# Kernel optimization log

Measured on AMD Instinct MI355X. Metric: run time of the kernel, lower is better.

The kernel has to match this reference:

```python
import jax, jax.numpy as jnp
import numpy as np

N, D, K, P = 4096, 256, 16, 3
MAXDEG = K + 1          # self loop guarantees deg >= 1, randint caps deg <= K+1
TAU, LAM, BETA, MARGIN = 0.8, 0.5, 1.0, 0.1
EPS_PD = 1e-6           # F.pairwise_distance eps (added to the difference)


def _make_adj(k):
    nbr = jax.random.randint(k, (N, K), 0, N)
    m = jnp.zeros((N, N), jnp.float32)
    m = m.at[jnp.arange(N)[:, None], nbr].set(1.0)
    m = m.at[jnp.arange(N), jnp.arange(N)].set(1.0)
    return m / m.sum(1, keepdims=True)  # row-normalized metapath adjacency


def setup_inputs():
    key = jax.random.key(0)
    ks = jax.random.split(key, 12)
    g = 1.414 * (2.0 / (D + D)) ** 0.5  # xavier_normal gain=1.414
    return {
        "h": jax.random.normal(ks[0], (N, D), jnp.float32),
        "mps": jnp.stack([_make_adj(ks[1 + i]) for i in range(P)]),
        "W_gcn": jax.random.normal(ks[4], (P, D, D), jnp.float32) * g,
        "b_gcn": jnp.zeros((P, D), jnp.float32),
        "prelu_a": jnp.full((P,), 0.25, jnp.float32),
        "att_fc_W": jax.random.normal(ks[5], (D, D), jnp.float32) * g,
        "att_fc_b": jnp.zeros((D,), jnp.float32),
        "att_vec": jax.random.normal(ks[6], (D,), jnp.float32) * g,
        "proj_W1": jax.random.normal(ks[7], (D, D), jnp.float32) * g,
        "proj_b1": jnp.zeros((D,), jnp.float32),
        "proj_W2": jax.random.normal(ks[8], (D, D), jnp.float32) * g,
        "proj_b2": jnp.zeros((D,), jnp.float32),
    }


def _gcn(h, adj, W, b, a):
    out = adj @ (h @ W.T) + b          # spmm(adj, fc(h)) + bias
    return jnp.where(out > 0, out, a * out)  # PReLU


def _node_loss(emb, adj):
    # vectorized form of the per-node nonzero/pairwise_distance loop
    mask = adj > 0                      # [N, N]
    deg = mask.sum(1)                   # [N], >= 1 via self loops
    # stable argsort: neighbors first (ascending index), matching torch.nonzero order
    pos_idx = jnp.argsort(~mask, axis=1)[:, :MAXDEG]
    neg_idx = jnp.argsort(mask, axis=1)[:, :MAXDEG]   # first deg non-neighbors
    anc = emb[:, None, :]               # anchor expanded over pairs
    dp = jnp.sum((anc - emb[pos_idx] + EPS_PD) ** 2, -1)  # [N, MAXDEG]
    dn = jnp.sum((anc - emb[neg_idx] + EPS_PD) ** 2, -1)
    valid = jnp.arange(MAXDEG)[None, :] < deg[:, None]
    per = jnp.maximum(dp - dn + MARGIN, 0.0) * valid
    return jnp.sum(per.sum(1) / deg.astype(emb.dtype))  # per-node mean, summed


def _proj(z, W1, b1, W2, b2):
    return jax.nn.elu(z @ W1.T + b1) @ W2.T + b2


def _contrast(z1, z2, pos, W1, b1, W2, b2):
    p1 = _proj(z1, W1, b1, W2, b2)
    p2 = _proj(z2, W1, b1, W2, b2)
    n1 = jnp.linalg.norm(p1, axis=-1, keepdims=True)
    n2 = jnp.linalg.norm(p2, axis=-1, keepdims=True)
    sim = jnp.exp((p1 @ p2.T) / (n1 * n2.T) / TAU)     # [N, N]
    m12 = sim / (sim.sum(1, keepdims=True) + 1e-8)
    m21 = sim.T / (sim.T.sum(1, keepdims=True) + 1e-8)
    l12 = -jnp.log((m12 * pos).sum(-1)).mean()
    l21 = -jnp.log((m21 * pos).sum(-1)).mean()
    return LAM * l12 + (1.0 - LAM) * l21


def reference(h, mps, W_gcn, b_gcn, prelu_a, att_fc_W, att_fc_b, att_vec,
              proj_W1, proj_b1, proj_W2, proj_b2):
    embeds = [_gcn(h, mps[i], W_gcn[i], b_gcn[i], prelu_a[i]) for i in range(P)]
    node_loss = sum(_node_loss(embeds[i], mps[i]) for i in range(P))
    # faithful to original control flow: i==0 inner loop overwrites self.loss,
    # so only the (0, P-1) pair survives from i==0
    closs = _contrast(embeds[0], embeds[P - 1], mps[0], proj_W1, proj_b1, proj_W2, proj_b2)
    for i in range(1, P - 1):
        for j in range(i + 1, P):
            closs = closs + _contrast(embeds[i], embeds[j], mps[i], proj_W1, proj_b1, proj_W2, proj_b2)
    # semantic attention over metapaths
    sp = jnp.stack([jnp.tanh(e @ att_fc_W.T + att_fc_b).mean(0) for e in embeds])  # [P, D]
    beta = jax.nn.softmax(sp @ att_vec)                                            # [P]
    z_mp = jnp.einsum('p,pnd->nd', beta, jnp.stack(embeds))
    return z_mp, node_loss + BETA * closs
```

## Files before the change

kernel.cpp:

```cpp
#include <hip/hip_runtime.h>
#include <hip/hip_bf16.h>

constexpr int N = 4096;
constexpr int D = 256;
constexpr int P = 3;
constexpr int MAXDEG = 17;
constexpr float TAU = 0.8f;
constexpr float MARGIN = 0.1f;
constexpr float EPS_PD = 1e-6f;

constexpr int LDP = 40;

constexpr int OFF_H    = 0;
constexpr int OFF_WG   = 1048576;
constexpr int OFF_ATTW = 1245184;
constexpr int OFF_W1   = 1310720;
constexpr int OFF_W2   = 1376256;
constexpr int OFF_BG   = 1441792;
constexpr int OFF_ATTB = 1442560;
constexpr int OFF_AV   = 1442816;
constexpr int OFF_PA   = 1443072;
constexpr int OFF_B1   = 1443328;
constexpr int OFF_B2   = 1443584;
constexpr int CONV_TOTAL = 1443840;

typedef __attribute__((ext_vector_type(8))) short bfrag8;
typedef __attribute__((ext_vector_type(4))) float facc4;

__device__ inline facc4 mfma16(bfrag8 a, bfrag8 b, facc4 c) {
    return __builtin_amdgcn_mfma_f32_16x16x32_bf16(a, b, c, 0, 0, 0);
}
__device__ inline float b2f(__hip_bfloat16 v) { return __bfloat162float(v); }
__device__ inline float bfbits2f(unsigned short u) {
    return __uint_as_float(((unsigned int)u) << 16);
}
__device__ inline unsigned short f2bfbits(float v) {
    __hip_bfloat16 t = __float2bfloat16(v);
    return *(unsigned short*)&t;
}
__device__ inline int get_bf(const int* __restrict__ counter) { return counter[0] > 100; }

__device__ inline float load_in(const void* p, size_t i, int bf) {
    return bf ? __bfloat162float(((const __hip_bfloat16*)p)[i])
              : ((const float*)p)[i];
}

__device__ __forceinline__ void gl_lds16(const __hip_bfloat16* g, __hip_bfloat16* l) {
    __builtin_amdgcn_global_load_lds(
        (const __attribute__((address_space(1))) unsigned int*)g,
        (__attribute__((address_space(3))) unsigned int*)l, 16, 0, 0);
}

__global__ void detect_dtype(const unsigned int* __restrict__ w, int nwords,
                             int* __restrict__ counter,
                             float* __restrict__ zbuf, int nz) {
    int t0 = blockIdx.x * blockDim.x + threadIdx.x;
    if (t0 < nz) zbuf[t0] = 0.f;
    int stride = gridDim.x * blockDim.x;
    int c = 0;
    for (int i = t0; i < nwords; i += stride) {
        unsigned int x = w[i];
        if ((x & 0xFFFF0000u) == 0u && x != 0u) c++;
    }
    for (int s = 32; s > 0; s >>= 1) c += __shfl_down(c, s);
    if ((threadIdx.x & 63) == 0 && c > 0) atomicMax(counter, 1 << 20);
}

__global__ void convert_all(const void* h, const void* wg, const void* attw,
                            const void* w1, const void* w2, const void* bg,
                            const void* attb, const void* av, const void* pa,
                            const void* b1, const void* b2,
                            const int* __restrict__ counter,
                            __hip_bfloat16* __restrict__ dst) {
    int bf = get_bf(counter);
    const void* srcs[11] = {h, wg, attw, w1, w2, bg, attb, av, pa, b1, b2};
    const int offs[11] = {OFF_H, OFF_WG, OFF_ATTW, OFF_W1, OFF_W2, OFF_BG,
                          OFF_ATTB, OFF_AV, OFF_PA, OFF_B1, OFF_B2};
    const int lens[11] = {1048576, 196608, 65536, 65536, 65536, 768, 256, 256, 3, 256, 256};
    int stride = gridDim.x * blockDim.x;
    int t0 = blockIdx.x * blockDim.x + threadIdx.x;
    #pragma unroll
    for (int s = 0; s < 11; s++) {
        for (int i = t0; i < lens[s]; i += stride)
            dst[offs[s] + i] = __float2bfloat16(load_in(srcs[s], i, bf));
    }
}

__global__ void extract_sparse(const void* __restrict__ mps, const int* __restrict__ counter,
                               int* __restrict__ nbr_idx, float* __restrict__ nbr_val,
                               int* __restrict__ neg_idx, int* __restrict__ deg) {
    int bf = get_bf(counter);
    int row = blockIdx.x;
    int t = threadIdx.x;
    __shared__ int cnt;
    __shared__ int sidx[32];
    __shared__ float sval[32];
    if (t == 0) cnt = 0;
    __syncthreads();
    int e0 = t * 16;
    if (bf) {
        const uint4* base = (const uint4*)((const __hip_bfloat16*)mps + (size_t)row * N + e0);
        #pragma unroll
        for (int v = 0; v < 2; v++) {
            uint4 w = base[v];
            unsigned int ws[4] = {w.x, w.y, w.z, w.w};
            #pragma unroll
            for (int j = 0; j < 4; j++) {
                unsigned short lo = (unsigned short)(ws[j] & 0xFFFFu);
                unsigned short hi = (unsigned short)(ws[j] >> 16);
                if (lo) { int k = atomicAdd(&cnt, 1); if (k < 32) { sidx[k] = e0 + v * 8 + j * 2;     sval[k] = bfbits2f(lo); } }
                if (hi) { int k = atomicAdd(&cnt, 1); if (k < 32) { sidx[k] = e0 + v * 8 + j * 2 + 1; sval[k] = bfbits2f(hi); } }
            }
        }
    } else {
        const float4* base = (const float4*)((const float*)mps + (size_t)row * N + e0);
        #pragma unroll
        for (int v = 0; v < 4; v++) {
            float4 w = base[v];
            float ws[4] = {w.x, w.y, w.z, w.w};
            #pragma unroll
            for (int j = 0; j < 4; j++)
                if (ws[j] > 0.f) { int k = atomicAdd(&cnt, 1); if (k < 32) { sidx[k] = e0 + v * 4 + j; sval[k] = ws[j]; } }
        }
    }
    __syncthreads();
    if (t < 64) {
        int dg = cnt; if (dg > MAXDEG) dg = MAXDEG;
        int myidx = 0; float myval = 0.f; int rank = 0;
        if (t < dg) {
            myidx = sidx[t]; myval = sval[t];
            for (int j = 0; j < dg; j++) rank += (sidx[j] < myidx) ? 1 : 0;
        }
        if (t < dg) { sidx[rank] = myidx; sval[rank] = myval; }
        if (t < MAXDEG) {
            nbr_idx[(size_t)row * MAXDEG + t] = (t < dg) ? sidx[t] : 0;
            nbr_val[(size_t)row * MAXDEG + t] = (t < dg) ? sval[t] : 0.f;
        }
        if (t == 0) deg[row] = dg;
        int c = t;
        bool cand = (c < dg + MAXDEG);
        bool isnbr = false;
        if (cand) for (int j = 0; j < dg; j++) isnbr |= (sidx[j] == c);
        bool nonnbr = cand && !isnbr;
        unsigned long long m = __ballot(nonnbr);
        int nrank = __popcll(m & ((c < 64) ? ((1ull << c) - 1ull) : ~0ull));
        if (nonnbr && nrank < MAXDEG) neg_idx[(size_t)row * MAXDEG + nrank] = c;
    }
}

__global__ void gemm_triple(const __hip_bfloat16* __restrict__ conv,
                            __hip_bfloat16* __restrict__ xbuf) {
    const __hip_bfloat16* A = conv + OFF_H;
    __shared__ __align__(16) __hip_bfloat16 As[64 * LDP];
    __shared__ __align__(16) __hip_bfloat16 Bs[3][64 * LDP];
    int bm = blockIdx.x * 64, bn = blockIdx.y * 64;
    int tid = threadIdx.x, wave = tid >> 6, lane = tid & 63;
    int quad = lane >> 4, l15 = lane & 15;
    int wr = (wave & 1) * 32, wc = (wave >> 1) * 32;
    facc4 acc[3][2][2] = {};
    int sr = tid >> 2, kq = (tid & 3) * 8;
    for (int k0 = 0; k0 < D; k0 += 32) {
        *(bfrag8*)&As[sr * LDP + kq] = *(const bfrag8*)&A[(size_t)(bm + sr) * D + k0 + kq];
        #pragma unroll
        for (int z = 0; z < 3; z++)
            *(bfrag8*)&Bs[z][sr * LDP + kq] =
                *(const bfrag8*)&conv[OFF_WG + (size_t)z * D * D + (size_t)(bn + sr) * D + k0 + kq];
        __syncthreads();
        bfrag8 af[2];
        #pragma unroll
        for (int mi = 0; mi < 2; mi++)
            af[mi] = *(const bfrag8*)&As[(wr + mi * 16 + l15) * LDP + quad * 8];
        #pragma unroll
        for (int z = 0; z < 3; z++) {
            bfrag8 bfr[2];
            #pragma unroll
            for (int ni = 0; ni < 2; ni++)
                bfr[ni] = *(const bfrag8*)&Bs[z][(wc + ni * 16 + l15) * LDP + quad * 8];
            #pragma unroll
            for (int mi = 0; mi < 2; mi++)
                #pragma unroll
                for (int ni = 0; ni < 2; ni++)
                    acc[z][mi][ni] = mfma16(af[mi], bfr[ni], acc[z][mi][ni]);
        }
        __syncthreads();
    }
    #pragma unroll
    for (int z = 0; z < 3; z++)
        #pragma unroll
        for (int mi = 0; mi < 2; mi++)
            #pragma unroll
            for (int ni = 0; ni < 2; ni++) {
                int col = bn + wc + ni * 16 + l15;
                #pragma unroll
                for (int r = 0; r < 4; r++) {
                    int row = bm + wr + mi * 16 + quad * 4 + r;
                    xbuf[(size_t)z * N * D + (size_t)row * D + col] =
                        __float2bfloat16(acc[z][mi][ni][r]);
                }
            }
}

__global__ void gemm_dual(const __hip_bfloat16* __restrict__ embBase,
                          const __hip_bfloat16* __restrict__ conv,
                          __hip_bfloat16* __restrict__ xbuf,
                          float* __restrict__ spacc) {
    int z = blockIdx.z;
    const __hip_bfloat16* A = embBase + (size_t)z * N * D;
    const __hip_bfloat16* Ba = conv + OFF_ATTW;
    const __hip_bfloat16* Bw = conv + OFF_W1;
    __shared__ __align__(16) __hip_bfloat16 As[64 * LDP];
    __shared__ __align__(16) __hip_bfloat16 Bsa[64 * LDP];
    __shared__ __align__(16) __hip_bfloat16 Bsw[64 * LDP];
    int bm = blockIdx.x * 64, bn = blockIdx.y * 64;
    int tid = threadIdx.x, wave = tid >> 6, lane = tid & 63;
    int quad = lane >> 4, l15 = lane & 15;
    int wr = (wave & 1) * 32, wc = (wave >> 1) * 32;
    facc4 accA[2][2] = {};
    facc4 accW[2][2] = {};
    int sr = tid >> 2, kq = (tid & 3) * 8;
    for (int k0 = 0; k0 < D; k0 += 32) {
        *(bfrag8*)&As[sr * LDP + kq]  = *(const bfrag8*)&A[(size_t)(bm + sr) * D + k0 + kq];
        *(bfrag8*)&Bsa[sr * LDP + kq] = *(const bfrag8*)&Ba[(size_t)(bn + sr) * D + k0 + kq];
        *(bfrag8*)&Bsw[sr * LDP + kq] = *(const bfrag8*)&Bw[(size_t)(bn + sr) * D + k0 + kq];
        __syncthreads();
        bfrag8 af[2], ba[2], bw[2];
        #pragma unroll
        for (int mi = 0; mi < 2; mi++)
            af[mi] = *(const bfrag8*)&As[(wr + mi * 16 + l15) * LDP + quad * 8];
        #pragma unroll
        for (int ni = 0; ni < 2; ni++) {
            ba[ni] = *(const bfrag8*)&Bsa[(wc + ni * 16 + l15) * LDP + quad * 8];
            bw[ni] = *(const bfrag8*)&Bsw[(wc + ni * 16 + l15) * LDP + quad * 8];
        }
        #pragma unroll
        for (int mi = 0; mi < 2; mi++)
            #pragma unroll
            for (int ni = 0; ni < 2; ni++) {
                accA[mi][ni] = mfma16(af[mi], ba[ni], accA[mi][ni]);
                accW[mi][ni] = mfma16(af[mi], bw[ni], accW[mi][ni]);
            }
        __syncthreads();
    }
    float cs[2] = {0.f, 0.f};
    #pragma unroll
    for (int mi = 0; mi < 2; mi++) {
        #pragma unroll
        for (int ni = 0; ni < 2; ni++) {
            int col = bn + wc + ni * 16 + l15;
            float battb = b2f(conv[OFF_ATTB + col]);
            float bb1   = b2f(conv[OFF_B1 + col]);
            #pragma unroll
            for (int r = 0; r < 4; r++) {
                int row = bm + wr + mi * 16 + quad * 4 + r;
                cs[ni] += tanhf(accA[mi][ni][r] + battb);
                float v = accW[mi][ni][r] + bb1;
                v = v > 0.f ? v : expm1f(v);
                xbuf[(size_t)z * N * D + (size_t)row * D + col] = __float2bfloat16(v);
            }
        }
    }
    #pragma unroll
    for (int ni = 0; ni < 2; ni++) {
        float v = cs[ni];
        v += __shfl_xor(v, 16); v += __shfl_xor(v, 32);
        if (quad == 0) {
            int col = bn + wc + ni * 16 + l15;
            atomicAdd(&spacc[(size_t)z * D + col], v);
        }
    }
}

__global__ void gemm_w2_norm(const __hip_bfloat16* __restrict__ xbase,
                             const __hip_bfloat16* __restrict__ conv,
                             __hip_bfloat16* __restrict__ qbase) {
    int z = blockIdx.z;
    const __hip_bfloat16* A = xbase + (size_t)z * N * D;
    const __hip_bfloat16* B = conv + OFF_W2;
    __shared__ __align__(16) __hip_bfloat16 As[16 * LDP];
    __shared__ __align__(16) __hip_bfloat16 Bs[256 * LDP];
    __shared__ float sred[4][16];
    int bm = blockIdx.x * 16;
    int tid = threadIdx.x, wave = tid >> 6, lane = tid & 63;
    int quad = lane >> 4, l15 = lane & 15;
    int wc = wave * 64;
    facc4 acc[4] = {};
    for (int k0 = 0; k0 < D; k0 += 32) {
        if (tid < 64) {
            int r = tid >> 2, kq = (tid & 3) * 8;
            *(bfrag8*)&As[r * LDP + kq] = *(const bfrag8*)&A[(size_t)(bm + r) * D + k0 + kq];
        }
        #pragma unroll
        for (int i = 0; i < 4; i++) {
            int f = tid + 256 * i;
            int r = f >> 2, kq = (f & 3) * 8;
            *(bfrag8*)&Bs[r * LDP + kq] = *(const bfrag8*)&B[(size_t)r * D + k0 + kq];
        }
        __syncthreads();
        bfrag8 af = *(const bfrag8*)&As[l15 * LDP + quad * 8];
        #pragma unroll
        for (int ni = 0; ni < 4; ni++) {
            bfrag8 bf = *(const bfrag8*)&Bs[(wc + ni * 16 + l15) * LDP + quad * 8];
            acc[ni] = mfma16(af, bf, acc[ni]);
        }
        __syncthreads();
    }
    float vv[4][4];
    #pragma unroll
    for (int ni = 0; ni < 4; ni++) {
        float bb = b2f(conv[OFF_B2 + wc + ni * 16 + l15]);
        #pragma unroll
        for (int r = 0; r < 4; r++) vv[ni][r] = acc[ni][r] + bb;
    }
    #pragma unroll
    for (int r = 0; r < 4; r++) {
        float ss = vv[0][r] * vv[0][r] + vv[1][r] * vv[1][r] +
                   vv[2][r] * vv[2][r] + vv[3][r] * vv[3][r];
        ss += __shfl_xor(ss, 1); ss += __shfl_xor(ss, 2);
        ss += __shfl_xor(ss, 4); ss += __shfl_xor(ss, 8);
        if (l15 == 0) sred[wave][quad * 4 + r] = ss;
    }
    __syncthreads();
    #pragma unroll
    for (int r = 0; r < 4; r++) {
        int rl = quad * 4 + r;
        float ssum = sred[0][rl] + sred[1][rl] + sred[2][rl] + sred[3][rl];
        float inv = rsqrtf(ssum + 1e-30f);
        int row = bm + rl;
        #pragma unroll
        for (int ni = 0; ni < 4; ni++)
            qbase[(size_t)z * N * D + (size_t)row * D + wc + ni * 16 + l15] =
                __float2bfloat16(vv[ni][r] * inv);
    }
}

__global__ void spmm_prelu(const __hip_bfloat16* __restrict__ Xbase,
                           const int* __restrict__ nbr_idx, const float* __restrict__ nbr_val,
                           const int* __restrict__ deg, const __hip_bfloat16* __restrict__ conv,
                           __hip_bfloat16* __restrict__ embBase) {
    int z = blockIdx.z;
    int wave = threadIdx.x >> 6, lane = threadIdx.x & 63;
    int n = blockIdx.x * 4 + wave;
    const __hip_bfloat16* X = Xbase + (size_t)z * N * D;
    int dg = deg[z * N + n];
    int idxv = 0; float valv = 0.f;
    if (lane < MAXDEG) {
        idxv = nbr_idx[((size_t)z * N + n) * MAXDEG + lane];
        valv = nbr_val[((size_t)z * N + n) * MAXDEG + lane];
    }
    float acc[4] = {0.f, 0.f, 0.f, 0.f};
    int k = 0;
    for (; k + 3 < dg; k += 4) {
        int j0 = __shfl(idxv, k), j1 = __shfl(idxv, k + 1);
        int j2 = __shfl(idxv, k + 2), j3 = __shfl(idxv, k + 3);
        float v0 = __shfl(valv, k), v1 = __shfl(valv, k + 1);
        float v2 = __shfl(valv, k + 2), v3 = __shfl(valv, k + 3);
        ushort4 x0 = *(const ushort4*)&X[(size_t)j0 * D + lane * 4];
        ushort4 x1 = *(const ushort4*)&X[(size_t)j1 * D + lane * 4];
        ushort4 x2 = *(const ushort4*)&X[(size_t)j2 * D + lane * 4];
        ushort4 x3 = *(const ushort4*)&X[(size_t)j3 * D + lane * 4];
        acc[0] += v0 * bfbits2f(x0.x) + v1 * bfbits2f(x1.x) + v2 * bfbits2f(x2.x) + v3 * bfbits2f(x3.x);
        acc[1] += v0 * bfbits2f(x0.y) + v1 * bfbits2f(x1.y) + v2 * bfbits2f(x2.y) + v3 * bfbits2f(x3.y);
        acc[2] += v0 * bfbits2f(x0.z) + v1 * bfbits2f(x1.z) + v2 * bfbits2f(x2.z) + v3 * bfbits2f(x3.z);
        acc[3] += v0 * bfbits2f(x0.w) + v1 * bfbits2f(x1.w) + v2 * bfbits2f(x2.w) + v3 * bfbits2f(x3.w);
    }
    for (; k < dg; k++) {
        int j0 = __shfl(idxv, k); float v0 = __shfl(valv, k);
        ushort4 x0 = *(const ushort4*)&X[(size_t)j0 * D + lane * 4];
        acc[0] += v0 * bfbits2f(x0.x); acc[1] += v0 * bfbits2f(x0.y);
        acc[2] += v0 * bfbits2f(x0.z); acc[3] += v0 * bfbits2f(x0.w);
    }
    ushort4 bb = *(const ushort4*)&conv[OFF_BG + z * D + lane * 4];
    float a = b2f(conv[OFF_PA + z]);
    ushort4 o;
    float v0 = acc[0] + bfbits2f(bb.x); o.x = f2bfbits(v0 > 0.f ? v0 : a * v0);
    float v1 = acc[1] + bfbits2f(bb.y); o.y = f2bfbits(v1 > 0.f ? v1 : a * v1);
    float v2 = acc[2] + bfbits2f(bb.z); o.z = f2bfbits(v2 > 0.f ? v2 : a * v2);
    float v3 = acc[3] + bfbits2f(bb.w); o.w = f2bfbits(v3 > 0.f ? v3 : a * v3);
    *(ushort4*)&embBase[(size_t)z * N * D + (size_t)n * D + lane * 4] = o;
}

__global__ void sim_mfma(const __hip_bfloat16* __restrict__ q,
                         float* __restrict__ rowsum, float* __restrict__ colsum) {
    int pair = blockIdx.z;
    const __hip_bfloat16* Qa = q + (size_t)pair * N * D;
    const __hip_bfloat16* Qb = q + (size_t)2 * N * D;
    __shared__ __align__(16) __hip_bfloat16 As[128 * 64];
    __shared__ __align__(16) __hip_bfloat16 Bs[128 * 64];
    int bm = blockIdx.x * 128, bn = blockIdx.y * 128;
    int tid = threadIdx.x, wave = tid >> 6, lane = tid & 63;
    int quad = lane >> 4, l15 = lane & 15;
    int wr = (wave & 1) * 64, wc = (wave >> 1) * 64;
    facc4 acc[4][4] = {};
    int sr0 = tid >> 3;
    int cc  = tid & 7;
    for (int k0 = 0; k0 < D; k0 += 64) {
        #pragma unroll
        for (int i = 0; i < 4; i++) {
            int r = sr0 + 32 * i;
            int cg = (cc ^ (r & 7)) * 8;
            gl_lds16(&Qa[(size_t)(bm + r) * D + k0 + cg], &As[r * 64 + cc * 8]);
            gl_lds16(&Qb[(size_t)(bn + r) * D + k0 + cg], &Bs[r * 64 + cc * 8]);
        }
        __syncthreads();
        #pragma unroll
        for (int kk = 0; kk < 64; kk += 32) {
            int kb = kk >> 3;
            bfrag8 af[4], bfr[4];
            #pragma unroll
            for (int mi = 0; mi < 4; mi++) {
                int R = wr + mi * 16 + l15;
                int pc = ((kb + quad) ^ (l15 & 7)) * 8;
                af[mi] = *(const bfrag8*)&As[R * 64 + pc];
            }
            #pragma unroll
            for (int ni = 0; ni < 4; ni++) {
                int R = wc + ni * 16 + l15;
                int pc = ((kb + quad) ^ (l15 & 7)) * 8;
                bfr[ni] = *(const bfrag8*)&Bs[R * 64 + pc];
            }
            #pragma unroll
            for (int mi = 0; mi < 4; mi++)
                #pragma unroll
                for (int ni = 0; ni < 4; ni++)
                    acc[mi][ni] = mfma16(af[mi], bfr[ni], acc[mi][ni]);
        }
        __syncthreads();
    }
    constexpr float invtau = 1.0f / TAU;
    float rs[4][4];
    float cs[4] = {0.f, 0.f, 0.f, 0.f};
    #pragma unroll
    for (int mi = 0; mi < 4; mi++)
        #pragma unroll
        for (int r = 0; r < 4; r++) rs[mi][r] = 0.f;
    #pragma unroll
    for (int mi = 0; mi < 4; mi++)
        #pragma unroll
        for (int ni = 0; ni < 4; ni++)
            #pragma unroll
            for (int r = 0; r < 4; r++) {
                float e = __expf(acc[mi][ni][r] * invtau);
                rs[mi][r] += e;
                cs[ni] += e;
            }
    #pragma unroll
    for (int mi = 0; mi < 4; mi++)
        #pragma unroll
        for (int r = 0; r < 4; r++) {
            float v = rs[mi][r];
            v += __shfl_xor(v, 1); v += __shfl_xor(v, 2);
            v += __shfl_xor(v, 4); v += __shfl_xor(v, 8);
            rs[mi][r] = v;
        }
    if (l15 == 0) {
        #pragma unroll
        for (int mi = 0; mi < 4; mi++)
            #pragma unroll
            for (int r = 0; r < 4; r++)
                atomicAdd(&rowsum[(size_t)pair * N + bm + wr + mi * 16 + quad * 4 + r], rs[mi][r]);
    }
    #pragma unroll
    for (int ni = 0; ni < 4; ni++) {
        float v = cs[ni];
        v += __shfl_xor(v, 16); v += __shfl_xor(v, 32);
        if (quad == 0)
            atomicAdd(&colsum[(size_t)pair * N + bn + wc + ni * 16 + l15], v);
    }
}

__global__ void edge_losses(const __hip_bfloat16* __restrict__ embBase,
                            const __hip_bfloat16* __restrict__ q,
                            const int* __restrict__ nbr_idx, const float* __restrict__ nbr_val,
                            const int* __restrict__ neg_idx, const int* __restrict__ deg,
                            float* __restrict__ nlpart,
                            float* __restrict__ pdrow, float* __restrict__ pdcol) {
    int z = blockIdx.z;
    int wave = threadIdx.x >> 6, lane = threadIdx.x & 63;
    int n = blockIdx.x * 4 + wave;
    if (z < P) {
        const __hip_bfloat16* emb = embBase + (size_t)z * N * D;
        int dg = deg[z * N + n];
        int ipv = 0, igv = 0;
        if (lane < MAXDEG) {
            ipv = nbr_idx[((size_t)z * N + n) * MAXDEG + lane];
            igv = neg_idx[((size_t)z * N + n) * MAXDEG + lane];
        }
        ushort4 ar = *(const ushort4*)&emb[(size_t)n * D + lane * 4];
        float a[4] = {bfbits2f(ar.x), bfbits2f(ar.y), bfbits2f(ar.z), bfbits2f(ar.w)};
        float s = 0.f;
        int k = 0;
        for (; k + 1 < dg; k += 2) {
            int jp0 = __shfl(ipv, k), jn0 = __shfl(igv, k);
            int jp1 = __shfl(ipv, k + 1), jn1 = __shfl(igv, k + 1);
            ushort4 pr0 = *(const ushort4*)&emb[(size_t)jp0 * D + lane * 4];
            ushort4 nr0 = *(const ushort4*)&emb[(size_t)jn0 * D + lane * 4];
            ushort4 pr1 = *(const ushort4*)&emb[(size_t)jp1 * D + lane * 4];
            ushort4 nr1 = *(const ushort4*)&emb[(size_t)jn1 * D + lane * 4];
            float dp0, dn0, dp1, dn1;
            {
                float x0 = a[0] - bfbits2f(pr0.x) + EPS_PD, y0 = a[0] - bfbits2f(nr0.x) + EPS_PD;
                float x1 = a[1] - bfbits2f(pr0.y) + EPS_PD, y1 = a[1] - bfbits2f(nr0.y) + EPS_PD;
                float x2 = a[2] - bfbits2f(pr0.z) + EPS_PD, y2 = a[2] - bfbits2f(nr0.z) + EPS_PD;
                float x3 = a[3] - bfbits2f(pr0.w) + EPS_PD, y3 = a[3] - bfbits2f(nr0.w) + EPS_PD;
                dp0 = x0 * x0 + x1 * x1 + x2 * x2 + x3 * x3;
                dn0 = y0 * y0 + y1 * y1 + y2 * y2 + y3 * y3;
            }
            {
                float x0 = a[0] - bfbits2f(pr1.x) + EPS_PD, y0 = a[0] - bfbits2f(nr1.x) + EPS_PD;
                float x1 = a[1] - bfbits2f(pr1.y) + EPS_PD, y1 = a[1] - bfbits2f(nr1.y) + EPS_PD;
                float x2 = a[2] - bfbits2f(pr1.z) + EPS_PD, y2 = a[2] - bfbits2f(nr1.z) + EPS_PD;
                float x3 = a[3] - bfbits2f(pr1.w) + EPS_PD, y3 = a[3] - bfbits2f(nr1.w) + EPS_PD;
                dp1 = x0 * x0 + x1 * x1 + x2 * x2 + x3 * x3;
                dn1 = y0 * y0 + y1 * y1 + y2 * y2 + y3 * y3;
            }
            #pragma unroll
            for (int st = 1; st <= 32; st <<= 1) {
                dp0 += __shfl_xor(dp0, st); dn0 += __shfl_xor(dn0, st);
                dp1 += __shfl_xor(dp1, st); dn1 += __shfl_xor(dn1, st);
            }
            float v0 = dp0 - dn0 + MARGIN; s += v0 > 0.f ? v0 : 0.f;
            float v1 = dp1 - dn1 + MARGIN; s += v1 > 0.f ? v1 : 0.f;
        }
        if (k < dg) {
            int jp = __shfl(ipv, k), jn = __shfl(igv, k);
            ushort4 pr = *(const ushort4*)&emb[(size_t)jp * D + lane * 4];
            ushort4 nr = *(const ushort4*)&emb[(size_t)jn * D + lane * 4];
            float x0 = a[0] - bfbits2f(pr.x) + EPS_PD, y0 = a[0] - bfbits2f(nr.x) + EPS_PD;
            float x1 = a[1] - bfbits2f(pr.y) + EPS_PD, y1 = a[1] - bfbits2f(nr.y) + EPS_PD;
            float x2 = a[2] - bfbits2f(pr.z) + EPS_PD, y2 = a[2] - bfbits2f(nr.z) + EPS_PD;
            float x3 = a[3] - bfbits2f(pr.w) + EPS_PD, y3 = a[3] - bfbits2f(nr.w) + EPS_PD;
            float dp = x0 * x0 + x1 * x1 + x2 * x2 + x3 * x3;
            float dn = y0 * y0 + y1 * y1 + y2 * y2 + y3 * y3;
            #pragma unroll
            for (int st = 1; st <= 32; st <<= 1) { dp += __shfl_xor(dp, st); dn += __shfl_xor(dn, st); }
            float v = dp - dn + MARGIN;
            s += v > 0.f ? v : 0.f;
        }
        if (lane == 0) nlpart[z * N + n] = s / (float)dg;
    } else {
        int pair = z - P;
        const __hip_bfloat16* Qa = q + (size_t)pair * N * D;
        const __hip_bfloat16* Qb = q + (size_t)2 * N * D;
        int dg = deg[pair * N + n];
        int idxv = 0; float valv = 0.f;
        if (lane < MAXDEG) {
            idxv = nbr_idx[((size_t)pair * N + n) * MAXDEG + lane];
            valv = nbr_val[((size_t)pair * N + n) * MAXDEG + lane];
        }
        const float invtau = 1.0f / TAU;
        ushort4 ar = *(const ushort4*)&Qa[(size_t)n * D + lane * 4];
        ushort4 br = *(const ushort4*)&Qb[(size_t)n * D + lane * 4];
        float a[4] = {bfbits2f(ar.x), bfbits2f(ar.y), bfbits2f(ar.z), bfbits2f(ar.w)};
        float b[4] = {bfbits2f(br.x), bfbits2f(br.y), bfbits2f(br.z), bfbits2f(br.w)};
        float sr = 0.f, sc = 0.f;
        int k = 0;
        for (; k + 1 < dg; k += 2) {
            int j0 = __shfl(idxv, k), j1 = __shfl(idxv, k + 1);
            float vk0 = __shfl(valv, k), vk1 = __shfl(valv, k + 1);
            ushort4 pj0 = *(const ushort4*)&Qb[(size_t)j0 * D + lane * 4];
            ushort4 aj0 = *(const ushort4*)&Qa[(size_t)j0 * D + lane * 4];
            ushort4 pj1 = *(const ushort4*)&Qb[(size_t)j1 * D + lane * 4];
            ushort4 aj1 = *(const ushort4*)&Qa[(size_t)j1 * D + lane * 4];
            float dr0 = a[0] * bfbits2f(pj0.x) + a[1] * bfbits2f(pj0.y) +
                        a[2] * bfbits2f(pj0.z) + a[3] * bfbits2f(pj0.w);
            float dc0 = b[0] * bfbits2f(aj0.x) + b[1] * bfbits2f(aj0.y) +
                        b[2] * bfbits2f(aj0.z) + b[3] * bfbits2f(aj0.w);
            float dr1 = a[0] * bfbits2f(pj1.x) + a[1] * bfbits2f(pj1.y) +
                        a[2] * bfbits2f(pj1.z) + a[3] * bfbits2f(pj1.w);
            float dc1 = b[0] * bfbits2f(aj1.x) + b[1] * bfbits2f(aj1.y) +
                        b[2] * bfbits2f(aj1.z) + b[3] * bfbits2f(aj1.w);
            #pragma unroll
            for (int s2 = 1; s2 <= 32; s2 <<= 1) {
                dr0 += __shfl_xor(dr0, s2); dc0 += __shfl_xor(dc0, s2);
                dr1 += __shfl_xor(dr1, s2); dc1 += __shfl_xor(dc1, s2);
            }
            sr += __expf(dr0 * invtau) * vk0 + __expf(dr1 * invtau) * vk1;
            sc += __expf(dc0 * invtau) * vk0 + __expf(dc1 * invtau) * vk1;
        }
        if (k < dg) {
            int j = __shfl(idxv, k);
            float vk = __shfl(valv, k);
            ushort4 pj = *(const ushort4*)&Qb[(size_t)j * D + lane * 4];
            ushort4 aj = *(const ushort4*)&Qa[(size_t)j * D + lane * 4];
            float dr = a[0] * bfbits2f(pj.x) + a[1] * bfbits2f(pj.y) +
                       a[2] * bfbits2f(pj.z) + a[3] * bfbits2f(pj.w);
            float dc = b[0] * bfbits2f(aj.x) + b[1] * bfbits2f(aj.y) +
                       b[2] * bfbits2f(aj.z) + b[3] * bfbits2f(aj.w);
            #pragma unroll
            for (int s2 = 1; s2 <= 32; s2 <<= 1) { dr += __shfl_xor(dr, s2); dc += __shfl_xor(dc, s2); }
            sr += __expf(dr * invtau) * vk;
            sc += __expf(dc * invtau) * vk;
        }
        if (lane == 0) { pdrow[pair * N + n] = sr; pdcol[pair * N + n] = sc; }
    }
}

__global__ void finalize(const float* __restrict__ nlpart,
                         const float* __restrict__ rowsum, const float* __restrict__ colsum,
                         const float* __restrict__ pdrow, const float* __restrict__ pdcol,
                         const float* __restrict__ spacc,
                         const __hip_bfloat16* __restrict__ conv,
                         const __hip_bfloat16* __restrict__ embBase,
                         const int* __restrict__ counter,
                         void* __restrict__ out) {
    int bf = get_bf(counter);
    int t = threadIdx.x;
    __shared__ float red[256];
    if (blockIdx.x == 0) {
        float s = 0.f;
        for (int i = t; i < P * N; i += 256) s += nlpart[i];
        for (int i = t; i < 2 * N; i += 256) {
            float l12 = -logf(pdrow[i] / (rowsum[i] + 1e-8f));
            float l21 = -logf(pdcol[i] / (colsum[i] + 1e-8f));
            s += (0.5f * l12 + 0.5f * l21) / (float)N;
        }
        red[t] = s;
        __syncthreads();
        for (int st = 128; st > 0; st >>= 1) { if (t < st) red[t] += red[t + st]; __syncthreads(); }
        if (t == 0) {
            if (bf) ((__hip_bfloat16*)out)[(size_t)N * D] = __float2bfloat16(red[0]);
            else    ((float*)out)[(size_t)N * D] = red[0];
        }
        return;
    }
    __shared__ float w[P];
    for (int p = 0; p < P; p++) {
        float v = (spacc[p * D + t] / (float)N) * b2f(conv[OFF_AV + t]);
        red[t] = v;
        __syncthreads();
        for (int s = 128; s > 0; s >>= 1) { if (t < s) red[t] += red[t + s]; __syncthreads(); }
        if (t == 0) w[p] = red[0];
        __syncthreads();
    }
    float m = fmaxf(w[0], fmaxf(w[1], w[2]));
    float e0 = __expf(w[0] - m), e1 = __expf(w[1] - m), e2 = __expf(w[2] - m);
    float ssum = e0 + e1 + e2;
    float b0 = e0 / ssum, b1 = e1 / ssum, b2 = e2 / ssum;
    int slice = blockIdx.x - 1;
    int base = slice * (N * D / 64);
    for (int e = t * 4; e < N * D / 64; e += 256 * 4) {
        int i = base + e;
        ushort4 x0 = *(const ushort4*)&embBase[i];
        ushort4 x1 = *(const ushort4*)&embBase[(size_t)N * D + i];
        ushort4 x2 = *(const ushort4*)&embBase[(size_t)2 * N * D + i];
        float v[4];
        v[0] = b0 * bfbits2f(x0.x) + b1 * bfbits2f(x1.x) + b2 * bfbits2f(x2.x);
        v[1] = b0 * bfbits2f(x0.y) + b1 * bfbits2f(x1.y) + b2 * bfbits2f(x2.y);
        v[2] = b0 * bfbits2f(x0.z) + b1 * bfbits2f(x1.z) + b2 * bfbits2f(x2.z);
        v[3] = b0 * bfbits2f(x0.w) + b1 * bfbits2f(x1.w) + b2 * bfbits2f(x2.w);
        if (bf) {
            ushort4 ov;
            ov.x = f2bfbits(v[0]); ov.y = f2bfbits(v[1]);
            ov.z = f2bfbits(v[2]); ov.w = f2bfbits(v[3]);
            *(ushort4*)&((__hip_bfloat16*)out)[i] = ov;
        } else {
            float* o = (float*)out;
            o[i] = v[0]; o[i + 1] = v[1]; o[i + 2] = v[2]; o[i + 3] = v[3];
        }
    }
}

extern "C" void kernel_launch(void* const* d_in, const int* in_sizes, int n_in,
                              void* d_out, int out_size, void* d_ws, size_t ws_size,
                              hipStream_t stream) {
    const void* h        = d_in[0];
    const void* mps      = d_in[1];
    const void* W_gcn    = d_in[2];
    const void* b_gcn    = d_in[3];
    const void* prelu_a  = d_in[4];
    const void* att_fc_W = d_in[5];
    const void* att_fc_b = d_in[6];
    const void* att_vec  = d_in[7];
    const void* proj_W1  = d_in[8];
    const void* proj_b1  = d_in[9];
    const void* proj_W2  = d_in[10];
    const void* proj_b2  = d_in[11];

    char* ws = (char*)d_ws;
    size_t off = 0;
    auto alloc = [&](size_t bytes) -> char* {
        char* p = ws + off;
        off = (off + bytes + 255) & ~(size_t)255;
        return p;
    };
    __hip_bfloat16* conv = (__hip_bfloat16*)alloc((size_t)CONV_TOTAL * 2);
    __hip_bfloat16* xbuf = (__hip_bfloat16*)alloc((size_t)P * N * D * 2);
    __hip_bfloat16* emb  = (__hip_bfloat16*)alloc((size_t)P * N * D * 2);
    __hip_bfloat16* q    = (__hip_bfloat16*)alloc((size_t)P * N * D * 2);
    int*   nbr_idx = (int*)alloc((size_t)P * N * MAXDEG * 4);
    float* nbr_val = (float*)alloc((size_t)P * N * MAXDEG * 4);
    int*   neg_idx = (int*)alloc((size_t)P * N * MAXDEG * 4);
    int*   deg     = (int*)alloc((size_t)P * N * 4);
    float* nlpart  = (float*)alloc((size_t)P * N * 4);
    float* pdrow   = (float*)alloc((size_t)2 * N * 4);
    float* pdcol   = (float*)alloc((size_t)2 * N * 4);
    char* zero_begin = ws + off;
    float* rowsum = (float*)alloc((size_t)2 * N * 4);
    float* colsum = (float*)alloc((size_t)2 * N * 4);
    float* spacc  = (float*)alloc((size_t)P * D * 4);
    size_t zero_bytes = (size_t)((ws + off) - zero_begin);
    int*   counter = (int*)alloc(16);

    detect_dtype<<<1024, 256, 0, stream>>>((const unsigned int*)mps, 2 * 1024 * 1024,
                                           counter, (float*)zero_begin,
                                           (int)(zero_bytes / 4));

    convert_all<<<512, 256, 0, stream>>>(h, W_gcn, att_fc_W, proj_W1, proj_W2, b_gcn,
                                         att_fc_b, att_vec, prelu_a, proj_b1, proj_b2,
                                         counter, conv);

    extract_sparse<<<P * N, 256, 0, stream>>>(mps, counter, nbr_idx, nbr_val, neg_idx, deg);

    gemm_triple<<<dim3(N / 64, D / 64), 256, 0, stream>>>(conv, xbuf);
    spmm_prelu<<<dim3(N / 4, 1, P), 256, 0, stream>>>(xbuf, nbr_idx, nbr_val, deg, conv, emb);
    gemm_dual<<<dim3(N / 64, D / 64, P), 256, 0, stream>>>(emb, conv, xbuf, spacc);
    gemm_w2_norm<<<dim3(N / 16, 1, P), 256, 0, stream>>>(xbuf, conv, q);
    sim_mfma<<<dim3(N / 128, N / 128, 2), 256, 0, stream>>>(q, rowsum, colsum);
    edge_losses<<<dim3(N / 4, 1, P + 2), 256, 0, stream>>>(emb, q, nbr_idx, nbr_val,
                                                           neg_idx, deg, nlpart, pdrow, pdcol);
    finalize<<<65, 256, 0, stream>>>(nlpart, rowsum, colsum, pdrow, pdcol,
                                     spacc, conv, emb, counter, d_out);
}
```

Baseline: 472.2 us.

## Fuse independent stages into shared launches to cut kernel count

The standalone convert pass is removed. The first GEMM now reads h and W_gcn directly and converts fp32 to bf16 on the fly, and it runs in the same launch as the sparse-extraction blocks using blockIdx ranges. The node-loss computation moves into the dual GEMM launch as extra blocks. The similarity GEMM, positive-pair sums and z_mp mixing are merged into one launch, leaving a small loss-finalize kernel. This removes several launches and inter-kernel bubbles and lets independent work overlap, at the cost of heterogeneous blocks with shared-memory sizing set by the largest branch.

```diff
diff --git a/kernel.cpp b/kernel.cpp
--- a/kernel.cpp
+++ b/kernel.cpp
@@ -66,270 +66,161 @@
     if ((threadIdx.x & 63) == 0 && c > 0) atomicMax(counter, 1 << 20);
 }
 
-__global__ void convert_all(const void* h, const void* wg, const void* attw,
-                            const void* w1, const void* w2, const void* bg,
-                            const void* attb, const void* av, const void* pa,
-                            const void* b1, const void* b2,
-                            const int* __restrict__ counter,
-                            __hip_bfloat16* __restrict__ dst) {
-    int bf = get_bf(counter);
-    const void* srcs[11] = {h, wg, attw, w1, w2, bg, attb, av, pa, b1, b2};
-    const int offs[11] = {OFF_H, OFF_WG, OFF_ATTW, OFF_W1, OFF_W2, OFF_BG,
-                          OFF_ATTB, OFF_AV, OFF_PA, OFF_B1, OFF_B2};
-    const int lens[11] = {1048576, 196608, 65536, 65536, 65536, 768, 256, 256, 3, 256, 256};
-    int stride = gridDim.x * blockDim.x;
-    int t0 = blockIdx.x * blockDim.x + threadIdx.x;
-    #pragma unroll
-    for (int s = 0; s < 11; s++) {
-        for (int i = t0; i < lens[s]; i += stride)
-            dst[offs[s] + i] = __float2bfloat16(load_in(srcs[s], i, bf));
-    }
-}
-
-__global__ void extract_sparse(const void* __restrict__ mps, const int* __restrict__ counter,
-                               int* __restrict__ nbr_idx, float* __restrict__ nbr_val,
-                               int* __restrict__ neg_idx, int* __restrict__ deg) {
-    int bf = get_bf(counter);
-    int row = blockIdx.x;
-    int t = threadIdx.x;
-    __shared__ int cnt;
-    __shared__ int sidx[32];
-    __shared__ float sval[32];
-    if (t == 0) cnt = 0;
-    __syncthreads();
-    int e0 = t * 16;
-    if (bf) {
-        const uint4* base = (const uint4*)((const __hip_bfloat16*)mps + (size_t)row * N + e0);
-        #pragma unroll
-        for (int v = 0; v < 2; v++) {
-            uint4 w = base[v];
-            unsigned int ws[4] = {w.x, w.y, w.z, w.w};
-            #pragma unroll
-            for (int j = 0; j < 4; j++) {
-                unsigned short lo = (unsigned short)(ws[j] & 0xFFFFu);
-                unsigned short hi = (unsigned short)(ws[j] >> 16);
-                if (lo) { int k = atomicAdd(&cnt, 1); if (k < 32) { sidx[k] = e0 + v * 8 + j * 2;     sval[k] = bfbits2f(lo); } }
-                if (hi) { int k = atomicAdd(&cnt, 1); if (k < 32) { sidx[k] = e0 + v * 8 + j * 2 + 1; sval[k] = bfbits2f(hi); } }
-            }
-        }
-    } else {
-        const float4* base = (const float4*)((const float*)mps + (size_t)row * N + e0);
-        #pragma unroll
-        for (int v = 0; v < 4; v++) {
-            float4 w = base[v];
-            float ws[4] = {w.x, w.y, w.z, w.w};
-            #pragma unroll
-            for (int j = 0; j < 4; j++)
-                if (ws[j] > 0.f) { int k = atomicAdd(&cnt, 1); if (k < 32) { sidx[k] = e0 + v * 4 + j; sval[k] = ws[j]; } }
-        }
-    }
-    __syncthreads();
-    if (t < 64) {
-        int dg = cnt; if (dg > MAXDEG) dg = MAXDEG;
-        int myidx = 0; float myval = 0.f; int rank = 0;
-        if (t < dg) {
-            myidx = sidx[t]; myval = sval[t];
-            for (int j = 0; j < dg; j++) rank += (sidx[j] < myidx) ? 1 : 0;
-        }
-        if (t < dg) { sidx[rank] = myidx; sval[rank] = myval; }
-        if (t < MAXDEG) {
-            nbr_idx[(size_t)row * MAXDEG + t] = (t < dg) ? sidx[t] : 0;
-            nbr_val[(size_t)row * MAXDEG + t] = (t < dg) ? sval[t] : 0.f;
-        }
-        if (t == 0) deg[row] = dg;
-        int c = t;
-        bool cand = (c < dg + MAXDEG);
-        bool isnbr = false;
-        if (cand) for (int j = 0; j < dg; j++) isnbr |= (sidx[j] == c);
-        bool nonnbr = cand && !isnbr;
-        unsigned long long m = __ballot(nonnbr);
-        int nrank = __popcll(m & ((c < 64) ? ((1ull << c) - 1ull) : ~0ull));
-        if (nonnbr && nrank < MAXDEG) neg_idx[(size_t)row * MAXDEG + nrank] = c;
-    }
-}
-
-__global__ void gemm_triple(const __hip_bfloat16* __restrict__ conv,
-                            __hip_bfloat16* __restrict__ xbuf) {
-    const __hip_bfloat16* A = conv + OFF_H;
+__global__ void stage2(const void* __restrict__ h, const void* __restrict__ wg,
+                       const void* __restrict__ mps,
+                       const void* attw, const void* w1, const void* w2,
+                       const void* bg, const void* attb, const void* av,
+                       const void* pa, const void* b1, const void* b2,
+                       const int* __restrict__ counter,
+                       __hip_bfloat16* __restrict__ conv,
+                       __hip_bfloat16* __restrict__ xbuf,
+                       int* __restrict__ nbr_idx, float* __restrict__ nbr_val,
+                       int* __restrict__ neg_idx, int* __restrict__ deg) {
     __shared__ __align__(16) __hip_bfloat16 As[64 * LDP];
     __shared__ __align__(16) __hip_bfloat16 Bs[3][64 * LDP];
-    int bm = blockIdx.x * 64, bn = blockIdx.y * 64;
-    int tid = threadIdx.x, wave = tid >> 6, lane = tid & 63;
-    int quad = lane >> 4, l15 = lane & 15;
-    int wr = (wave & 1) * 32, wc = (wave >> 1) * 32;
-    facc4 acc[3][2][2] = {};
-    int sr = tid >> 2, kq = (tid & 3) * 8;
-    for (int k0 = 0; k0 < D; k0 += 32) {
-        *(bfrag8*)&As[sr * LDP + kq] = *(const bfrag8*)&A[(size_t)(bm + sr) * D + k0 + kq];
+    int bid = blockIdx.x;
+    int bf = get_bf(counter);
+    if (bid < 256) {
+        int bm = (bid & 63) * 64, bn = (bid >> 6) * 64;
+        int tid = threadIdx.x, wave = tid >> 6, lane = tid & 63;
+        int quad = lane >> 4, l15 = lane & 15;
+        int wr = (wave & 1) * 32, wc = (wave >> 1) * 32;
+        facc4 acc[3][2][2] = {};
+        int sr = tid >> 2, kq = (tid & 3) * 8;
+        for (int k0 = 0; k0 < D; k0 += 32) {
+            if (bf) {
+                *(bfrag8*)&As[sr * LDP + kq] =
+                    *(const bfrag8*)((const unsigned short*)h + (size_t)(bm + sr) * D + k0 + kq);
+                #pragma unroll
+                for (int z = 0; z < 3; z++)
+                    *(bfrag8*)&Bs[z][sr * LDP + kq] =
+                        *(const bfrag8*)((const unsigned short*)wg +
+                                         (size_t)z * D * D + (size_t)(bn + sr) * D + k0 + kq);
+            } else {
+                const float* hp = (const float*)h + (size_t)(bm + sr) * D + k0 + kq;
+                float4 a0 = *(const float4*)hp, a1 = *(const float4*)(hp + 4);
+                bfrag8 t;
+                t[0] = f2bfbits(a0.x); t[1] = f2bfbits(a0.y);
+                t[2] = f2bfbits(a0.z); t[3] = f2bfbits(a0.w);
+                t[4] = f2bfbits(a1.x); t[5] = f2bfbits(a1.y);
+                t[6] = f2bfbits(a1.z); t[7] = f2bfbits(a1.w);
+                *(bfrag8*)&As[sr * LDP + kq] = t;
+                #pragma unroll
+                for (int z = 0; z < 3; z++) {
+                    const float* wp = (const float*)wg +
+                        (size_t)z * D * D + (size_t)(bn + sr) * D + k0 + kq;
+                    float4 b0 = *(const float4*)wp, b1v = *(const float4*)(wp + 4);
+                    bfrag8 u;
+                    u[0] = f2bfbits(b0.x);  u[1] = f2bfbits(b0.y);
+                    u[2] = f2bfbits(b0.z);  u[3] = f2bfbits(b0.w);
+                    u[4] = f2bfbits(b1v.x); u[5] = f2bfbits(b1v.y);
+                    u[6] = f2bfbits(b1v.z); u[7] = f2bfbits(b1v.w);
+                    *(bfrag8*)&Bs[z][sr * LDP + kq] = u;
+                }
+            }
+            __syncthreads();
+            bfrag8 af[2];
+            #pragma unroll
+            for (int mi = 0; mi < 2; mi++)
+                af[mi] = *(const bfrag8*)&As[(wr + mi * 16 + l15) * LDP + quad * 8];
+            #pragma unroll
+            for (int z = 0; z < 3; z++) {
+                bfrag8 bfr[2];
+                #pragma unroll
+                for (int ni = 0; ni < 2; ni++)
+                    bfr[ni] = *(const bfrag8*)&Bs[z][(wc + ni * 16 + l15) * LDP + quad * 8];
+                #pragma unroll
+                for (int mi = 0; mi < 2; mi++)
+                    #pragma unroll
+                    for (int ni = 0; ni < 2; ni++)
+                        acc[z][mi][ni] = mfma16(af[mi], bfr[ni], acc[z][mi][ni]);
+            }
+            __syncthreads();
+        }
         #pragma unroll
         for (int z = 0; z < 3; z++)
-            *(bfrag8*)&Bs[z][sr * LDP + kq] =
-                *(const bfrag8*)&conv[OFF_WG + (size_t)z * D * D + (size_t)(bn + sr) * D + k0 + kq];
+            #pragma unroll
+            for (int mi = 0; mi < 2; mi++)
+                #pragma unroll
+                for (int ni = 0; ni < 2; ni++) {
+                    int col = bn + wc + ni * 16 + l15;
+                    #pragma unroll
+                    for (int r = 0; r < 4; r++) {
+                        int row = bm + wr + mi * 16 + quad * 4 + r;
+                        xbuf[(size_t)z * N * D + (size_t)row * D + col] =
+                            __float2bfloat16(acc[z][mi][ni][r]);
+                    }
+                }
+    } else if (bid < 256 + P * N) {
+        int row = bid - 256;
+        int t = threadIdx.x;
+        int* cnt = (int*)As;
+        int* sidx = ((int*)As) + 1;
+        float* sval = (float*)(((int*)As) + 33);
+        if (t == 0) *cnt = 0;
         __syncthreads();
-        bfrag8 af[2];
-        #pragma unroll
-        for (int mi = 0; mi < 2; mi++)
-            af[mi] = *(const bfrag8*)&As[(wr + mi * 16 + l15) * LDP + quad * 8];
-        #pragma unroll
-        for (int z = 0; z < 3; z++) {
-            bfrag8 bfr[2];
-            #pragma unroll
-            for (int ni = 0; ni < 2; ni++)
-                bfr[ni] = *(const bfrag8*)&Bs[z][(wc + ni * 16 + l15) * LDP + quad * 8];
-            #pragma unroll
-            for (int mi = 0; mi < 2; mi++)
-                #pragma unroll
-                for (int ni = 0; ni < 2; ni++)
-                    acc[z][mi][ni] = mfma16(af[mi], bfr[ni], acc[z][mi][ni]);
+        int e0 = t * 16;
+        if (bf) {
+            const uint4* base = (const uint4*)((const __hip_bfloat16*)mps + (size_t)row * N + e0);
+            #pragma unroll
+            for (int v = 0; v < 2; v++) {
+                uint4 w = base[v];
+                unsigned int ws[4] = {w.x, w.y, w.z, w.w};
+                #pragma unroll
+                for (int j = 0; j < 4; j++) {
+                    unsigned short lo = (unsigned short)(ws[j] & 0xFFFFu);
+                    unsigned short hi = (unsigned short)(ws[j] >> 16);
+                    if (lo) { int k = atomicAdd(cnt, 1); if (k < 32) { sidx[k] = e0 + v * 8 + j * 2;     sval[k] = bfbits2f(lo); } }
+                    if (hi) { int k = atomicAdd(cnt, 1); if (k < 32) { sidx[k] = e0 + v * 8 + j * 2 + 1; sval[k] = bfbits2f(hi); } }
+                }
+            }
+        } else {
+            const float4* base = (const float4*)((const float*)mps + (size_t)row * N + e0);
+            #pragma unroll
+            for (int v = 0; v < 4; v++) {
+                float4 w = base[v];
+                float ws[4] = {w.x, w.y, w.z, w.w};
+                #pragma unroll
+                for (int j = 0; j < 4; j++)
+                    if (ws[j] > 0.f) { int k = atomicAdd(cnt, 1); if (k < 32) { sidx[k] = e0 + v * 4 + j; sval[k] = ws[j]; } }
+            }
         }
         __syncthreads();
-    }
-    #pragma unroll
-    for (int z = 0; z < 3; z++)
-        #pragma unroll
-        for (int mi = 0; mi < 2; mi++)
-            #pragma unroll
-            for (int ni = 0; ni < 2; ni++) {
-                int col = bn + wc + ni * 16 + l15;
-                #pragma unroll
-                for (int r = 0; r < 4; r++) {
-                    int row = bm + wr + mi * 16 + quad * 4 + r;
-                    xbuf[(size_t)z * N * D + (size_t)row * D + col] =
-                        __float2bfloat16(acc[z][mi][ni][r]);
-                }
-            }
-}
-
-__global__ void gemm_dual(const __hip_bfloat16* __restrict__ embBase,
-                          const __hip_bfloat16* __restrict__ conv,
-                          __hip_bfloat16* __restrict__ xbuf,
-                          float* __restrict__ spacc) {
-    int z = blockIdx.z;
-    const __hip_bfloat16* A = embBase + (size_t)z * N * D;
-    const __hip_bfloat16* Ba = conv + OFF_ATTW;
-    const __hip_bfloat16* Bw = conv + OFF_W1;
-    __shared__ __align__(16) __hip_bfloat16 As[64 * LDP];
-    __shared__ __align__(16) __hip_bfloat16 Bsa[64 * LDP];
-    __shared__ __align__(16) __hip_bfloat16 Bsw[64 * LDP];
-    int bm = blockIdx.x * 64, bn = blockIdx.y * 64;
-    int tid = threadIdx.x, wave = tid >> 6, lane = tid & 63;
-    int quad = lane >> 4, l15 = lane & 15;
-    int wr = (wave & 1) * 32, wc = (wave >> 1) * 32;
-    facc4 accA[2][2] = {};
-    facc4 accW[2][2] = {};
-    int sr = tid >> 2, kq = (tid & 3) * 8;
-    for (int k0 = 0; k0 < D; k0 += 32) {
-        *(bfrag8*)&As[sr * LDP + kq]  = *(const bfrag8*)&A[(size_t)(bm + sr) * D + k0 + kq];
-        *(bfrag8*)&Bsa[sr * LDP + kq] = *(const bfrag8*)&Ba[(size_t)(bn + sr) * D + k0 + kq];
-        *(bfrag8*)&Bsw[sr * LDP + kq] = *(const bfrag8*)&Bw[(size_t)(bn + sr) * D + k0 + kq];
-        __syncthreads();
-        bfrag8 af[2], ba[2], bw[2];
-        #pragma unroll
-        for (int mi = 0; mi < 2; mi++)
-            af[mi] = *(const bfrag8*)&As[(wr + mi * 16 + l15) * LDP + quad * 8];
-        #pragma unroll
-        for (int ni = 0; ni < 2; ni++) {
-            ba[ni] = *(const bfrag8*)&Bsa[(wc + ni * 16 + l15) * LDP + quad * 8];
-            bw[ni] = *(const bfrag8*)&Bsw[(wc + ni * 16 + l15) * LDP + quad * 8];
-        }
-        #pragma unroll
-        for (int mi = 0; mi < 2; mi++)
-            #pragma unroll
-            for (int ni = 0; ni < 2; ni++) {
-                accA[mi][ni] = mfma16(af[mi], ba[ni], accA[mi][ni]);
-                accW[mi][ni] = mfma16(af[mi], bw[ni], accW[mi][ni]);
-            }
-        __syncthreads();
-    }
-    float cs[2] = {0.f, 0.f};
-    #pragma unroll
-    for (int mi = 0; mi < 2; mi++) {
-        #pragma unroll
-        for (int ni = 0; ni < 2; ni++) {
-            int col = bn + wc + ni * 16 + l15;
-            float battb = b2f(conv[OFF_ATTB + col]);
-            float bb1   = b2f(conv[OFF_B1 + col]);
-            #pragma unroll
-            for (int r = 0; r < 4; r++) {
-                int row = bm + wr + mi * 16 + quad * 4 + r;
-                cs[ni] += tanhf(accA[mi][ni][r] + battb);
-                float v = accW[mi][ni][r] + bb1;
-                v = v > 0.f ? v : expm1f(v);
-                xbuf[(size_t)z * N * D + (size_t)row * D + col] = __float2bfloat16(v);
-            }
-        }
-    }
-    #pragma unroll
-    for (int ni = 0; ni < 2; ni++) {
-        float v = cs[ni];
-        v += __shfl_xor(v, 16); v += __shfl_xor(v, 32);
-        if (quad == 0) {
-            int col = bn + wc + ni * 16 + l15;
-            atomicAdd(&spacc[(size_t)z * D + col], v);
-        }
-    }
-}
-
-__global__ void gemm_w2_norm(const __hip_bfloat16* __restrict__ xbase,
-                             const __hip_bfloat16* __restrict__ conv,
-                             __hip_bfloat16* __restrict__ qbase) {
-    int z = blockIdx.z;
-    const __hip_bfloat16* A = xbase + (size_t)z * N * D;
-    const __hip_bfloat16* B = conv + OFF_W2;
-    __shared__ __align__(16) __hip_bfloat16 As[16 * LDP];
-    __shared__ __align__(16) __hip_bfloat16 Bs[256 * LDP];
-    __shared__ float sred[4][16];
-    int bm = blockIdx.x * 16;
-    int tid = threadIdx.x, wave = tid >> 6, lane = tid & 63;
-    int quad = lane >> 4, l15 = lane & 15;
-    int wc = wave * 64;
-    facc4 acc[4] = {};
-    for (int k0 = 0; k0 < D; k0 += 32) {
-        if (tid < 64) {
-            int r = tid >> 2, kq = (tid & 3) * 8;
-            *(bfrag8*)&As[r * LDP + kq] = *(const bfrag8*)&A[(size_t)(bm + r) * D + k0 + kq];
-        }
-        #pragma unroll
-        for (int i = 0; i < 4; i++) {
-            int f = tid + 256 * i;
-            int r = f >> 2, kq = (f & 3) * 8;
-            *(bfrag8*)&Bs[r * LDP + kq] = *(const bfrag8*)&B[(size_t)r * D + k0 + kq];
-        }
-        __syncthreads();
-        bfrag8 af = *(const bfrag8*)&As[l15 * LDP + quad * 8];
-        #pragma unroll
-        for (int ni = 0; ni < 4; ni++) {
-            bfrag8 bf = *(const bfrag8*)&Bs[(wc + ni * 16 + l15) * LDP + quad * 8];
-            acc[ni] = mfma16(af, bf, acc[ni]);
-        }
-        __syncthreads();
-    }
-    float vv[4][4];
-    #pragma unroll
-    for (int ni = 0; ni < 4; ni++) {
-        float bb = b2f(conv[OFF_B2 + wc + ni * 16 + l15]);
-        #pragma unroll
-        for (int r = 0; r < 4; r++) vv[ni][r] = acc[ni][r] + bb;
-    }
-    #pragma unroll
-    for (int r = 0; r < 4; r++) {
-        float ss = vv[0][r] * vv[0][r] + vv[1][r] * vv[1][r] +
-                   vv[2][r] * vv[2][r] + vv[3][r] * vv[3][r];
-        ss += __shfl_xor(ss, 1); ss += __shfl_xor(ss, 2);
-        ss += __shfl_xor(ss, 4); ss += __shfl_xor(ss, 8);
-        if (l15 == 0) sred[wave][quad * 4 + r] = ss;
-    }
-    __syncthreads();
-    #pragma unroll
-    for (int r = 0; r < 4; r++) {
-        int rl = quad * 4 + r;
-        float ssum = sred[0][rl] + sred[1][rl] + sred[2][rl] + sred[3][rl];
-        float inv = rsqrtf(ssum + 1e-30f);
-        int row = bm + rl;
-        #pragma unroll
-        for (int ni = 0; ni < 4; ni++)
-            qbase[(size_t)z * N * D + (size_t)row * D + wc + ni * 16 + l15] =
-                __float2bfloat16(vv[ni][r] * inv);
+        if (t < 64) {
+            int dg = *cnt; if (dg > MAXDEG) dg = MAXDEG;
+            int myidx = 0; float myval = 0.f; int rank = 0;
+            if (t < dg) {
+                myidx = sidx[t]; myval = sval[t];
+                for (int j = 0; j < dg; j++) rank += (sidx[j] < myidx) ? 1 : 0;
+            }
+            if (t < dg) { sidx[rank] = myidx; sval[rank] = myval; }
+            if (t < MAXDEG) {
+                nbr_idx[(size_t)row * MAXDEG + t] = (t < dg) ? sidx[t] : 0;
+                nbr_val[(size_t)row * MAXDEG + t] = (t < dg) ? sval[t] : 0.f;
+            }
+            if (t == 0) deg[row] = dg;
+            int c = t;
+            bool cand = (c < dg + MAXDEG);
+            bool isnbr = false;
+            if (cand) for (int j = 0; j < dg; j++) isnbr |= (sidx[j] == c);
+            bool nonnbr = cand && !isnbr;
+            unsigned long long m = __ballot(nonnbr);
+            int nrank = __popcll(m & ((c < 64) ? ((1ull << c) - 1ull) : ~0ull));
+            if (nonnbr && nrank < MAXDEG) neg_idx[(size_t)row * MAXDEG + nrank] = c;
+        }
+    } else {
+        int cb = bid - (256 + P * N);
+        const void* srcs[9] = {attw, w1, w2, bg, attb, av, pa, b1, b2};
+        const int offs[9] = {OFF_ATTW, OFF_W1, OFF_W2, OFF_BG, OFF_ATTB,
+                             OFF_AV, OFF_PA, OFF_B1, OFF_B2};
+        const int lens[9] = {65536, 65536, 65536, 768, 256, 256, 3, 256, 256};
+        int stride = 64 * 256;
+        int t0 = cb * 256 + threadIdx.x;
+        #pragma unroll
+        for (int s = 0; s < 9; s++) {
+            for (int i = t0; i < lens[s]; i += stride)
+                conv[offs[s] + i] = __float2bfloat16(load_in(srcs[s], i, bf));
+        }
     }
 }
 
@@ -379,105 +270,83 @@
     *(ushort4*)&embBase[(size_t)z * N * D + (size_t)n * D + lane * 4] = o;
 }
 
-__global__ void sim_mfma(const __hip_bfloat16* __restrict__ q,
-                         float* __restrict__ rowsum, float* __restrict__ colsum) {
-    int pair = blockIdx.z;
-    const __hip_bfloat16* Qa = q + (size_t)pair * N * D;
-    const __hip_bfloat16* Qb = q + (size_t)2 * N * D;
-    __shared__ __align__(16) __hip_bfloat16 As[128 * 64];
-    __shared__ __align__(16) __hip_bfloat16 Bs[128 * 64];
-    int bm = blockIdx.x * 128, bn = blockIdx.y * 128;
-    int tid = threadIdx.x, wave = tid >> 6, lane = tid & 63;
-    int quad = lane >> 4, l15 = lane & 15;
-    int wr = (wave & 1) * 64, wc = (wave >> 1) * 64;
-    facc4 acc[4][4] = {};
-    int sr0 = tid >> 3;
-    int cc  = tid & 7;
-    for (int k0 = 0; k0 < D; k0 += 64) {
-        #pragma unroll
-        for (int i = 0; i < 4; i++) {
-            int r = sr0 + 32 * i;
-            int cg = (cc ^ (r & 7)) * 8;
-            gl_lds16(&Qa[(size_t)(bm + r) * D + k0 + cg], &As[r * 64 + cc * 8]);
-            gl_lds16(&Qb[(size_t)(bn + r) * D + k0 + cg], &Bs[r * 64 + cc * 8]);
-        }
-        __syncthreads();
-        #pragma unroll
-        for (int kk = 0; kk < 64; kk += 32) {
-            int kb = kk >> 3;
-            bfrag8 af[4], bfr[4];
-            #pragma unroll
-            for (int mi = 0; mi < 4; mi++) {
-                int R = wr + mi * 16 + l15;
-                int pc = ((kb + quad) ^ (l15 & 7)) * 8;
-                af[mi] = *(const bfrag8*)&As[R * 64 + pc];
-            }
-            #pragma unroll
-            for (int ni = 0; ni < 4; ni++) {
-                int R = wc + ni * 16 + l15;
-                int pc = ((kb + quad) ^ (l15 & 7)) * 8;
-                bfr[ni] = *(const bfrag8*)&Bs[R * 64 + pc];
-            }
-            #pragma unroll
-            for (int mi = 0; mi < 4; mi++)
-                #pragma unroll
-                for (int ni = 0; ni < 4; ni++)
-                    acc[mi][ni] = mfma16(af[mi], bfr[ni], acc[mi][ni]);
-        }
-        __syncthreads();
-    }
-    constexpr float invtau = 1.0f / TAU;
-    float rs[4][4];
-    float cs[4] = {0.f, 0.f, 0.f, 0.f};
-    #pragma unroll
-    for (int mi = 0; mi < 4; mi++)
-        #pragma unroll
-        for (int r = 0; r < 4; r++) rs[mi][r] = 0.f;
-    #pragma unroll
-    for (int mi = 0; mi < 4; mi++)
-        #pragma unroll
-        for (int ni = 0; ni < 4; ni++)
-            #pragma unroll
-            for (int r = 0; r < 4; r++) {
-                float e = __expf(acc[mi][ni][r] * invtau);
-                rs[mi][r] += e;
-                cs[ni] += e;
-            }
-    #pragma unroll
-    for (int mi = 0; mi < 4; mi++)
-        #pragma unroll
-        for (int r = 0; r < 4; r++) {
-            float v = rs[mi][r];
-            v += __shfl_xor(v, 1); v += __shfl_xor(v, 2);
-            v += __shfl_xor(v, 4); v += __shfl_xor(v, 8);
-            rs[mi][r] = v;
-        }
-    if (l15 == 0) {
-        #pragma unroll
-        for (int mi = 0; mi < 4; mi++)
-            #pragma unroll
-            for (int r = 0; r < 4; r++)
-                atomicAdd(&rowsum[(size_t)pair * N + bm + wr + mi * 16 + quad * 4 + r], rs[mi][r]);
-    }
-    #pragma unroll
-    for (int ni = 0; ni < 4; ni++) {
-        float v = cs[ni];
-        v += __shfl_xor(v, 16); v += __shfl_xor(v, 32);
-        if (quad == 0)
-            atomicAdd(&colsum[(size_t)pair * N + bn + wc + ni * 16 + l15], v);
-    }
-}
-
-__global__ void edge_losses(const __hip_bfloat16* __restrict__ embBase,
-                            const __hip_bfloat16* __restrict__ q,
-                            const int* __restrict__ nbr_idx, const float* __restrict__ nbr_val,
-                            const int* __restrict__ neg_idx, const int* __restrict__ deg,
-                            float* __restrict__ nlpart,
-                            float* __restrict__ pdrow, float* __restrict__ pdcol) {
+__global__ void gemm_dual_nl(const __hip_bfloat16* __restrict__ embBase,
+                             const __hip_bfloat16* __restrict__ conv,
+                             __hip_bfloat16* __restrict__ xbuf,
+                             float* __restrict__ spacc,
+                             const int* __restrict__ nbr_idx,
+                             const int* __restrict__ neg_idx,
+                             const int* __restrict__ deg,
+                             float* __restrict__ nlpart) {
+    __shared__ __align__(16) __hip_bfloat16 As[64 * LDP];
+    __shared__ __align__(16) __hip_bfloat16 Bsa[64 * LDP];
+    __shared__ __align__(16) __hip_bfloat16 Bsw[64 * LDP];
     int z = blockIdx.z;
-    int wave = threadIdx.x >> 6, lane = threadIdx.x & 63;
-    int n = blockIdx.x * 4 + wave;
-    if (z < P) {
+    if (blockIdx.y < 4) {
+        const __hip_bfloat16* A = embBase + (size_t)z * N * D;
+        const __hip_bfloat16* Ba = conv + OFF_ATTW;
+        const __hip_bfloat16* Bw = conv + OFF_W1;
+        int bm = blockIdx.x * 64, bn = blockIdx.y * 64;
+        int tid = threadIdx.x, wave = tid >> 6, lane = tid & 63;
+        int quad = lane >> 4, l15 = lane & 15;
+        int wr = (wave & 1) * 32, wc = (wave >> 1) * 32;
+        facc4 accA[2][2] = {};
+        facc4 accW[2][2] = {};
+        int sr = tid >> 2, kq = (tid & 3) * 8;
+        for (int k0 = 0; k0 < D; k0 += 32) {
+            *(bfrag8*)&As[sr * LDP + kq]  = *(const bfrag8*)&A[(size_t)(bm + sr) * D + k0 + kq];
+            *(bfrag8*)&Bsa[sr * LDP + kq] = *(const bfrag8*)&Ba[(size_t)(bn + sr) * D + k0 + kq];
+            *(bfrag8*)&Bsw[sr * LDP + kq] = *(const bfrag8*)&Bw[(size_t)(bn + sr) * D + k0 + kq];
+            __syncthreads();
+            bfrag8 af[2], ba[2], bw[2];
+            #pragma unroll
+            for (int mi = 0; mi < 2; mi++)
+                af[mi] = *(const bfrag8*)&As[(wr + mi * 16 + l15) * LDP + quad * 8];
+            #pragma unroll
+            for (int ni = 0; ni < 2; ni++) {
+                ba[ni] = *(const bfrag8*)&Bsa[(wc + ni * 16 + l15) * LDP + quad * 8];
+                bw[ni] = *(const bfrag8*)&Bsw[(wc + ni * 16 + l15) * LDP + quad * 8];
+            }
+            #pragma unroll
+            for (int mi = 0; mi < 2; mi++)
+                #pragma unroll
+                for (int ni = 0; ni < 2; ni++) {
+                    accA[mi][ni] = mfma16(af[mi], ba[ni], accA[mi][ni]);
+                    accW[mi][ni] = mfma16(af[mi], bw[ni], accW[mi][ni]);
+                }
+            __syncthreads();
+        }
+        float cs[2] = {0.f, 0.f};
+        #pragma unroll
+        for (int mi = 0; mi < 2; mi++) {
+            #pragma unroll
+            for (int ni = 0; ni < 2; ni++) {
+                int col = bn + wc + ni * 16 + l15;
+                float battb = b2f(conv[OFF_ATTB + col]);
+                float bb1   = b2f(conv[OFF_B1 + col]);
+                #pragma unroll
+                for (int r = 0; r < 4; r++) {
+                    int row = bm + wr + mi * 16 + quad * 4 + r;
+                    cs[ni] += tanhf(accA[mi][ni][r] + battb);
+                    float v = accW[mi][ni][r] + bb1;
+                    v = v > 0.f ? v : expm1f(v);
+                    xbuf[(size_t)z * N * D + (size_t)row * D + col] = __float2bfloat16(v);
+                }
+            }
+        }
+        #pragma unroll
+        for (int ni = 0; ni < 2; ni++) {
+            float v = cs[ni];
+            v += __shfl_xor(v, 16); v += __shfl_xor(v, 32);
+            if (quad == 0) {
+                int col = bn + wc + ni * 16 + l15;
+                atomicAdd(&spacc[(size_t)z * D + col], v);
+            }
+        }
+    } else {
+        int wave = threadIdx.x >> 6, lane = threadIdx.x & 63;
+        int nb = blockIdx.x * 16 + (blockIdx.y - 4);
+        int n = nb * 4 + wave;
         const __hip_bfloat16* emb = embBase + (size_t)z * N * D;
         int dg = deg[z * N + n];
         int ipv = 0, igv = 0;
@@ -537,8 +406,173 @@
             s += v > 0.f ? v : 0.f;
         }
         if (lane == 0) nlpart[z * N + n] = s / (float)dg;
-    } else {
-        int pair = z - P;
+    }
+}
+
+__global__ void gemm_w2_norm(const __hip_bfloat16* __restrict__ xbase,
+                             const __hip_bfloat16* __restrict__ conv,
+                             __hip_bfloat16* __restrict__ qbase) {
+    int z = blockIdx.z;
+    const __hip_bfloat16* A = xbase + (size_t)z * N * D;
+    const __hip_bfloat16* B = conv + OFF_W2;
+    __shared__ __align__(16) __hip_bfloat16 As[16 * LDP];
+    __shared__ __align__(16) __hip_bfloat16 Bs[256 * LDP];
+    __shared__ float sred[4][16];
+    int bm = blockIdx.x * 16;
+    int tid = threadIdx.x, wave = tid >> 6, lane = tid & 63;
+    int quad = lane >> 4, l15 = lane & 15;
+    int wc = wave * 64;
+    facc4 acc[4] = {};
+    for (int k0 = 0; k0 < D; k0 += 32) {
+        if (tid < 64) {
+            int r = tid >> 2, kq = (tid & 3) * 8;
+            *(bfrag8*)&As[r * LDP + kq] = *(const bfrag8*)&A[(size_t)(bm + r) * D + k0 + kq];
+        }
+        #pragma unroll
+        for (int i = 0; i < 4; i++) {
+            int f = tid + 256 * i;
+            int r = f >> 2, kq = (f & 3) * 8;
+            *(bfrag8*)&Bs[r * LDP + kq] = *(const bfrag8*)&B[(size_t)r * D + k0 + kq];
+        }
+        __syncthreads();
+        bfrag8 af = *(const bfrag8*)&As[l15 * LDP + quad * 8];
+        #pragma unroll
+        for (int ni = 0; ni < 4; ni++) {
+            bfrag8 bf = *(const bfrag8*)&Bs[(wc + ni * 16 + l15) * LDP + quad * 8];
+            acc[ni] = mfma16(af, bf, acc[ni]);
+        }
+        __syncthreads();
+    }
+    float vv[4][4];
+    #pragma unroll
+    for (int ni = 0; ni < 4; ni++) {
+        float bb = b2f(conv[OFF_B2 + wc + ni * 16 + l15]);
+        #pragma unroll
+        for (int r = 0; r < 4; r++) vv[ni][r] = acc[ni][r] + bb;
+    }
+    #pragma unroll
+    for (int r = 0; r < 4; r++) {
+        float ss = vv[0][r] * vv[0][r] + vv[1][r] * vv[1][r] +
+                   vv[2][r] * vv[2][r] + vv[3][r] * vv[3][r];
+        ss += __shfl_xor(ss, 1); ss += __shfl_xor(ss, 2);
+        ss += __shfl_xor(ss, 4); ss += __shfl_xor(ss, 8);
+        if (l15 == 0) sred[wave][quad * 4 + r] = ss;
+    }
+    __syncthreads();
+    #pragma unroll
+    for (int r = 0; r < 4; r++) {
+        int rl = quad * 4 + r;
+        float ssum = sred[0][rl] + sred[1][rl] + sred[2][rl] + sred[3][rl];
+        float inv = rsqrtf(ssum + 1e-30f);
+        int row = bm + rl;
+        #pragma unroll
+        for (int ni = 0; ni < 4; ni++)
+            qbase[(size_t)z * N * D + (size_t)row * D + wc + ni * 16 + l15] =
+                __float2bfloat16(vv[ni][r] * inv);
+    }
+}
+
+__global__ void sim_pd_zmp(const __hip_bfloat16* __restrict__ q,
+                           float* __restrict__ rowsum, float* __restrict__ colsum,
+                           const __hip_bfloat16* __restrict__ embBase,
+                           const int* __restrict__ nbr_idx, const float* __restrict__ nbr_val,
+                           const int* __restrict__ deg,
+                           float* __restrict__ pdrow, float* __restrict__ pdcol,
+                           const float* __restrict__ spacc,
+                           const __hip_bfloat16* __restrict__ conv,
+                           const int* __restrict__ counter,
+                           void* __restrict__ out) {
+    __shared__ __align__(16) __hip_bfloat16 As[128 * 64];
+    __shared__ __align__(16) __hip_bfloat16 Bs[128 * 64];
+    int pair = blockIdx.z;
+    int y = blockIdx.y;
+    if (y < 32) {
+        const __hip_bfloat16* Qa = q + (size_t)pair * N * D;
+        const __hip_bfloat16* Qb = q + (size_t)2 * N * D;
+        int bm = blockIdx.x * 128, bn = y * 128;
+        int tid = threadIdx.x, wave = tid >> 6, lane = tid & 63;
+        int quad = lane >> 4, l15 = lane & 15;
+        int wr = (wave & 1) * 64, wc = (wave >> 1) * 64;
+        facc4 acc[4][4] = {};
+        int sr0 = tid >> 3;
+        int cc  = tid & 7;
+        for (int k0 = 0; k0 < D; k0 += 64) {
+            #pragma unroll
+            for (int i = 0; i < 4; i++) {
+                int r = sr0 + 32 * i;
+                int cg = (cc ^ (r & 7)) * 8;
+                gl_lds16(&Qa[(size_t)(bm + r) * D + k0 + cg], &As[r * 64 + cc * 8]);
+                gl_lds16(&Qb[(size_t)(bn + r) * D + k0 + cg], &Bs[r * 64 + cc * 8]);
+            }
+            __syncthreads();
+            #pragma unroll
+            for (int kk = 0; kk < 64; kk += 32) {
+                int kb = kk >> 3;
+                bfrag8 af[4], bfr[4];
+                #pragma unroll
+                for (int mi = 0; mi < 4; mi++) {
+                    int R = wr + mi * 16 + l15;
+                    int pc = ((kb + quad) ^ (l15 & 7)) * 8;
+                    af[mi] = *(const bfrag8*)&As[R * 64 + pc];
+                }
+                #pragma unroll
+                for (int ni = 0; ni < 4; ni++) {
+                    int R = wc + ni * 16 + l15;
+                    int pc = ((kb + quad) ^ (l15 & 7)) * 8;
+                    bfr[ni] = *(const bfrag8*)&Bs[R * 64 + pc];
+                }
+                #pragma unroll
+                for (int mi = 0; mi < 4; mi++)
+                    #pragma unroll
+                    for (int ni = 0; ni < 4; ni++)
+                        acc[mi][ni] = mfma16(af[mi], bfr[ni], acc[mi][ni]);
+            }
+            __syncthreads();
+        }
+        constexpr float invtau = 1.0f / TAU;
+        float rs[4][4];
+        float cs[4] = {0.f, 0.f, 0.f, 0.f};
+        #pragma unroll
+        for (int mi = 0; mi < 4; mi++)
+            #pragma unroll
+            for (int r = 0; r < 4; r++) rs[mi][r] = 0.f;
+        #pragma unroll
+        for (int mi = 0; mi < 4; mi++)
+            #pragma unroll
+            for (int ni = 0; ni < 4; ni++)
+                #pragma unroll
+                for (int r = 0; r < 4; r++) {
+                    float e = __expf(acc[mi][ni][r] * invtau);
+                    rs[mi][r] += e;
+                    cs[ni] += e;
+                }
+        #pragma unroll
+        for (int mi = 0; mi < 4; mi++)
+            #pragma unroll
+            for (int r = 0; r < 4; r++) {
+                float v = rs[mi][r];
+                v += __shfl_xor(v, 1); v += __shfl_xor(v, 2);
+                v += __shfl_xor(v, 4); v += __shfl_xor(v, 8);
+                rs[mi][r] = v;
+            }
+        if (l15 == 0) {
+            #pragma unroll
+            for (int mi = 0; mi < 4; mi++)
+                #pragma unroll
+                for (int r = 0; r < 4; r++)
+                    atomicAdd(&rowsum[(size_t)pair * N + bm + wr + mi * 16 + quad * 4 + r], rs[mi][r]);
+        }
+        #pragma unroll
+        for (int ni = 0; ni < 4; ni++) {
+            float v = cs[ni];
+            v += __shfl_xor(v, 16); v += __shfl_xor(v, 32);
+            if (quad == 0)
+                atomicAdd(&colsum[(size_t)pair * N + bn + wc + ni * 16 + l15], v);
+        }
+    } else if (y < 64) {
+        int wave = threadIdx.x >> 6, lane = threadIdx.x & 63;
+        int nb = blockIdx.x * 32 + (y - 32);
+        int n = nb * 4 + wave;
         const __hip_bfloat16* Qa = q + (size_t)pair * N * D;
         const __hip_bfloat16* Qb = q + (size_t)2 * N * D;
         int dg = deg[pair * N + n];
@@ -592,71 +626,69 @@
             sc += __expf(dc * invtau) * vk;
         }
         if (lane == 0) { pdrow[pair * N + n] = sr; pdcol[pair * N + n] = sc; }
-    }
-}
-
-__global__ void finalize(const float* __restrict__ nlpart,
-                         const float* __restrict__ rowsum, const float* __restrict__ colsum,
-                         const float* __restrict__ pdrow, const float* __restrict__ pdcol,
-                         const float* __restrict__ spacc,
-                         const __hip_bfloat16* __restrict__ conv,
-                         const __hip_bfloat16* __restrict__ embBase,
-                         const int* __restrict__ counter,
-                         void* __restrict__ out) {
+    } else {
+        int bf = get_bf(counter);
+        int t = threadIdx.x;
+        float* red = (float*)As;
+        float* w   = (float*)Bs;
+        for (int p = 0; p < P; p++) {
+            float v = (spacc[p * D + t] / (float)N) * b2f(conv[OFF_AV + t]);
+            red[t] = v;
+            __syncthreads();
+            for (int s = 128; s > 0; s >>= 1) { if (t < s) red[t] += red[t + s]; __syncthreads(); }
+            if (t == 0) w[p] = red[0];
+            __syncthreads();
+        }
+        float m = fmaxf(w[0], fmaxf(w[1], w[2]));
+        float e0 = __expf(w[0] - m), e1 = __expf(w[1] - m), e2 = __expf(w[2] - m);
+        float ssum = e0 + e1 + e2;
+        float b0 = e0 / ssum, b1 = e1 / ssum, b2 = e2 / ssum;
+        int slice = pair * 32 + blockIdx.x;
+        int base = slice * (N * D / 64);
+        for (int e = t * 4; e < N * D / 64; e += 256 * 4) {
+            int i = base + e;
+            ushort4 x0 = *(const ushort4*)&embBase[i];
+            ushort4 x1 = *(const ushort4*)&embBase[(size_t)N * D + i];
+            ushort4 x2 = *(const ushort4*)&embBase[(size_t)2 * N * D + i];
+            float v[4];
+            v[0] = b0 * bfbits2f(x0.x) + b1 * bfbits2f(x1.x) + b2 * bfbits2f(x2.x);
+            v[1] = b0 * bfbits2f(x0.y) + b1 * bfbits2f(x1.y) + b2 * bfbits2f(x2.y);
+            v[2] = b0 * bfbits2f(x0.z) + b1 * bfbits2f(x1.z) + b2 * bfbits2f(x2.z);
+            v[3] = b0 * bfbits2f(x0.w) + b1 * bfbits2f(x1.w) + b2 * bfbits2f(x2.w);
+            if (bf) {
+                ushort4 ov;
+                ov.x = f2bfbits(v[0]); ov.y = f2bfbits(v[1]);
+                ov.z = f2bfbits(v[2]); ov.w = f2bfbits(v[3]);
+                *(ushort4*)&((__hip_bfloat16*)out)[i] = ov;
+            } else {
+                float* o = (float*)out;
+                o[i] = v[0]; o[i + 1] = v[1]; o[i + 2] = v[2]; o[i + 3] = v[3];
+            }
+        }
+    }
+}
+
+__global__ void finalize_loss(const float* __restrict__ nlpart,
+                              const float* __restrict__ rowsum, const float* __restrict__ colsum,
+                              const float* __restrict__ pdrow, const float* __restrict__ pdcol,
+                              const int* __restrict__ counter,
+                              void* __restrict__ out) {
     int bf = get_bf(counter);
     int t = threadIdx.x;
     __shared__ float red[256];
-    if (blockIdx.x == 0) {
-        float s = 0.f;
-        for (int i = t; i < P * N; i += 256) s += nlpart[i];
-        for (int i = t; i < 2 * N; i += 256) {
-            float l12 = -logf(pdrow[i] / (rowsum[i] + 1e-8f));
-            float l21 = -logf(pdcol[i] / (colsum[i] + 1e-8f));
-            s += (0.5f * l12 + 0.5f * l21) / (float)N;
-        }
-        red[t] = s;
-        __syncthreads();
-        for (int st = 128; st > 0; st >>= 1) { if (t < st) red[t] += red[t + st]; __syncthreads(); }
-        if (t == 0) {
-            if (bf) ((__hip_bfloat16*)out)[(size_t)N * D] = __float2bfloat16(red[0]);
-            else    ((float*)out)[(size_t)N * D] = red[0];
-        }
-        return;
-    }
-    __shared__ float w[P];
-    for (int p = 0; p < P; p++) {
-        float v = (spacc[p * D + t] / (float)N) * b2f(conv[OFF_AV + t]);
-        red[t] = v;
-        __syncthreads();
-        for (int s = 128; s > 0; s >>= 1) { if (t < s) red[t] += red[t + s]; __syncthreads(); }
-        if (t == 0) w[p] = red[0];
-        __syncthreads();
-    }
-    float m = fmaxf(w[0], fmaxf(w[1], w[2]));
-    float e0 = __expf(w[0] - m), e1 = __expf(w[1] - m), e2 = __expf(w[2] - m);
-    float ssum = e0 + e1 + e2;
-    float b0 = e0 / ssum, b1 = e1 / ssum, b2 = e2 / ssum;
-    int slice = blockIdx.x - 1;
-    int base = slice * (N * D / 64);
-    for (int e = t * 4; e < N * D / 64; e += 256 * 4) {
-        int i = base + e;
-        ushort4 x0 = *(const ushort4*)&embBase[i];
-        ushort4 x1 = *(const ushort4*)&embBase[(size_t)N * D + i];
-        ushort4 x2 = *(const ushort4*)&embBase[(size_t)2 * N * D + i];
-        float v[4];
-        v[0] = b0 * bfbits2f(x0.x) + b1 * bfbits2f(x1.x) + b2 * bfbits2f(x2.x);
-        v[1] = b0 * bfbits2f(x0.y) + b1 * bfbits2f(x1.y) + b2 * bfbits2f(x2.y);
-        v[2] = b0 * bfbits2f(x0.z) + b1 * bfbits2f(x1.z) + b2 * bfbits2f(x2.z);
-        v[3] = b0 * bfbits2f(x0.w) + b1 * bfbits2f(x1.w) + b2 * bfbits2f(x2.w);
-        if (bf) {
-            ushort4 ov;
-            ov.x = f2bfbits(v[0]); ov.y = f2bfbits(v[1]);
-            ov.z = f2bfbits(v[2]); ov.w = f2bfbits(v[3]);
-            *(ushort4*)&((__hip_bfloat16*)out)[i] = ov;
-        } else {
-            float* o = (float*)out;
-            o[i] = v[0]; o[i + 1] = v[1]; o[i + 2] = v[2]; o[i + 3] = v[3];
-        }
+    float s = 0.f;
+    for (int i = t; i < P * N; i += 256) s += nlpart[i];
+    for (int i = t; i < 2 * N; i += 256) {
+        float l12 = -logf(pdrow[i] / (rowsum[i] + 1e-8f));
+        float l21 = -logf(pdcol[i] / (colsum[i] + 1e-8f));
+        s += (0.5f * l12 + 0.5f * l21) / (float)N;
+    }
+    red[t] = s;
+    __syncthreads();
+    for (int st = 128; st > 0; st >>= 1) { if (t < st) red[t] += red[t + st]; __syncthreads(); }
+    if (t == 0) {
+        if (bf) ((__hip_bfloat16*)out)[(size_t)N * D] = __float2bfloat16(red[0]);
+        else    ((float*)out)[(size_t)N * D] = red[0];
     }
 }
 
@@ -705,19 +737,24 @@
                                            counter, (float*)zero_begin,
                                            (int)(zero_bytes / 4));
 
-    convert_all<<<512, 256, 0, stream>>>(h, W_gcn, att_fc_W, proj_W1, proj_W2, b_gcn,
-                                         att_fc_b, att_vec, prelu_a, proj_b1, proj_b2,
-                                         counter, conv);
-
-    extract_sparse<<<P * N, 256, 0, stream>>>(mps, counter, nbr_idx, nbr_val, neg_idx, deg);
-
-    gemm_triple<<<dim3(N / 64, D / 64), 256, 0, stream>>>(conv, xbuf);
+    stage2<<<256 + P * N + 64, 256, 0, stream>>>(h, W_gcn, mps,
+                                                 att_fc_W, proj_W1, proj_W2, b_gcn,
+                                                 att_fc_b, att_vec, prelu_a, proj_b1, proj_b2,
+                                                 counter, conv, xbuf,
+                                                 nbr_idx, nbr_val, neg_idx, deg);
+
     spmm_prelu<<<dim3(N / 4, 1, P), 256, 0, stream>>>(xbuf, nbr_idx, nbr_val, deg, conv, emb);
-    gemm_dual<<<dim3(N / 64, D / 64, P), 256, 0, stream>>>(emb, conv, xbuf, spacc);
+
+    gemm_dual_nl<<<dim3(64, 20, P), 256, 0, stream>>>(emb, conv, xbuf, spacc,
+                                                      nbr_idx, neg_idx, deg, nlpart);
+
     gemm_w2_norm<<<dim3(N / 16, 1, P), 256, 0, stream>>>(xbuf, conv, q);
-    sim_mfma<<<dim3(N / 128, N / 128, 2), 256, 0, stream>>>(q, rowsum, colsum);
-    edge_losses<<<dim3(N / 4, 1, P + 2), 256, 0, stream>>>(emb, q, nbr_idx, nbr_val,
-                                                           neg_idx, deg, nlpart, pdrow, pdcol);
-    finalize<<<65, 256, 0, stream>>>(nlpart, rowsum, colsum, pdrow, pdcol,
-                                     spacc, conv, emb, counter, d_out);
-}
+
+    sim_pd_zmp<<<dim3(32, 65, 2), 256, 0, stream>>>(q, rowsum, colsum, emb,
+                                                    nbr_idx, nbr_val, deg,
+                                                    pdrow, pdcol, spacc, conv,
+                                                    counter, d_out);
+
+    finalize_loss<<<1, 256, 0, stream>>>(nlpart, rowsum, colsum, pdrow, pdcol,
+                                         counter, d_out);
+}
```

New measurement: 458.5 us. -2.9%, faster.
